# Kernel optimization log

Measured on AMD Instinct MI355X. Metric: run time of the kernel, lower is better.

## Reference

```python
import jax, jax.numpy as jnp
import numpy as np

EPS = 1e-5

def _bn(x, g, b, m, v):
    # eval-mode BatchNorm1d over channel dim of [B, C, T]
    scale = g / jnp.sqrt(v + EPS)
    return (x - m[:, None]) * scale[:, None] + b[:, None]

def _conv3(x, w, b):
    # [B, W, T] conv with kernel [W, W, 3], padding=1
    y = jax.lax.conv_general_dilated(x, w, (1,), [(1, 1)],
                                     dimension_numbers=('NCH', 'OIH', 'NCH'))
    return y + b[None, :, None]

def setup_inputs() -> dict:
    key = jax.random.key(0)
    ks = iter(jax.random.split(key, 32))
    def n(shape, s=0.05):
        return jax.random.normal(next(ks), shape, jnp.float32) * s
    def u(shape):
        return jax.random.uniform(next(ks), shape, jnp.float32, 0.5, 1.5)
    B, T, C, S, W = 128, 4096, 125, 5, 25
    return dict(
        low_freq=jax.random.normal(next(ks), (B, 10, T), jnp.float32),
        w1=n((S, W, 2)), b1=n((S, W)),
        w3=n((S - 1, W, W, 3)), b3=n((S - 1, W)),
        bn_g=jnp.ones((S, W)), bn_b=jnp.zeros((S, W)), bn_m=n((S, W)), bn_v=u((S, W)),
        gw1=n((C // 4, C)), gb1=n((C // 4,)),          # gating Linear(125, 31)
        gw2=n((S, C // 4)), gb2=n((S,)),               # gating Linear(31, 5)
        id_w=n((C, 10)), id_b=n((C,)),                 # identity_proj Conv1d(10,125,1)
        pf_w=n((C, C)), pf_b=n((C,)),                  # proj_final Conv1d(125,125,1)
        fbn_g=jnp.ones((C,)), fbn_b=jnp.zeros((C,)), fbn_m=n((C,)), fbn_v=u((C,)),
        ln_g=jnp.ones((C,)), ln_b=jnp.zeros((C,)),
        fc1_w=n((64, C)), fc1_b=n((64,)),
        fc2_w=n((2, 64)), fc2_b=n((2,)),
    )

def reference(low_freq, w1, b1, w3, b3, bn_g, bn_b, bn_m, bn_v,
              gw1, gb1, gw2, gb2, id_w, id_b, pf_w, pf_b,
              fbn_g, fbn_b, fbn_m, fbn_v, ln_g, ln_b,
              fc1_w, fc1_b, fc2_w, fc2_b):
    S = w1.shape[0]
    B, _, T = low_freq.shape
    identity = jnp.einsum('bct,oc->bot', low_freq, id_w) + id_b[None, :, None]
    chunks = low_freq.reshape(B, S, 2, T)              # torch.chunk over 10 channels
    # all 1x1 convs at once: [S, B, W, T]
    xs = jnp.einsum('bsct,swc->sbwt', chunks, w1) + b1[:, None, :, None]
    y = [None] * S
    y[S - 1] = jax.nn.relu(_bn(xs[S - 1], bn_g[S - 1], bn_b[S - 1], bn_m[S - 1], bn_v[S - 1]))
    for i in range(S - 2, -1, -1):                     # sequential Res2Net recursion
        yi = _conv3(xs[i] + y[i + 1], w3[i], b3[i])
        y[i] = jax.nn.relu(_bn(yi, bn_g[i], bn_b[i], bn_m[i], bn_v[i]))
    ms = jnp.concatenate(y, axis=1)                    # [B, 125, T]
    avg = jnp.mean(ms, axis=-1)                        # [B, 125]
    gate = jax.nn.sigmoid(jax.nn.relu(avg @ gw1.T + gb1) @ gw2.T + gb2)  # [B, S]
    yw = jnp.stack(y, axis=1) * gate[:, :, None, None] # [B, S, W, T]
    gated = yw.reshape(B, -1, T)
    proj = jnp.einsum('bct,oc->bot', gated, pf_w) + pf_b[None, :, None]
    out = jax.nn.relu(_bn(proj + identity, fbn_g, fbn_b, fbn_m, fbn_v))
    pooled = jnp.mean(out, axis=-1)                    # GAP -> [B, 125]
    mu = jnp.mean(pooled, axis=-1, keepdims=True)
    var = jnp.var(pooled, axis=-1, keepdims=True)
    normed = (pooled - mu) / jnp.sqrt(var + EPS) * ln_g + ln_b
    h = normed @ fc1_w.T + fc1_b
    h = jnp.where(h > 0, h, 0.2 * h)                   # LeakyReLU(0.2); dropout = identity (eval)
    return h @ fc2_w.T + fc2_b                         # [B, 2]
```

## Files before the change

kernel.cpp:

```cpp
#include <hip/hip_runtime.h>
#include <stdint.h>

typedef unsigned short u16;
typedef unsigned int   u32;
using short8 = __attribute__((ext_vector_type(8))) short;
using f32x4  = __attribute__((ext_vector_type(4))) float;

__device__ __forceinline__ u16 f2bf(float f){
  u32 u = __builtin_bit_cast(u32, f);
  u = u + 0x7fffu + ((u >> 16) & 1u);
  return (u16)(u >> 16);
}
__device__ __forceinline__ u32 packbf2(float a, float b){
  u32 ua = __builtin_bit_cast(u32, a) + 0x8000u;
  u32 ub = __builtin_bit_cast(u32, b) + 0x8000u;
  return (ua >> 16) | (ub & 0xffff0000u);
}

__global__ void prep_kernel(const float* __restrict__ w3,
                            const float* __restrict__ w1,
                            const float* __restrict__ b1,
                            const float* __restrict__ bng,
                            const float* __restrict__ bnv,
                            u16* __restrict__ convA)
{
  int idx = blockIdx.x*256 + threadIdx.x;
  if (idx >= 4*2*3*64*8) return;
  int j = idx & 7, l = (idx>>3) & 63, frag = idx >> 9;
  int tap = frag % 3, mt = (frag/3) & 1, lay = frag/6;
  int m = mt*16 + (l & 15);
  int k = (l>>4)*8 + j;
  float v = 0.f;
  if (m < 25){
    float a = bng[lay*25+m] * rsqrtf(bnv[lay*25+m] + 1e-5f);
    if (k < 25){
      v = a * w3[((lay*25+m)*25 + k)*3 + tap];
    } else if (k == 25){
      float s = 0.f;
      for (int c = 0; c < 25; ++c) s += w3[((lay*25+m)*25+c)*3+tap] * b1[lay*25+c];
      v = a * s;
    } else if (k <= 27){
      int e = k - 26;
      float s = 0.f;
      for (int c = 0; c < 25; ++c) s += w3[((lay*25+m)*25+c)*3+tap] * w1[(lay*25+c)*2+e];
      v = a * s;
    }
  }
  convA[idx] = f2bf(v);
}

template<int PASS, int CT>
__global__ __launch_bounds__(256, (PASS==1) ? 4 : 2)
void pass_kernel(const float* __restrict__ lfg,
                 const float* __restrict__ w1g, const float* __restrict__ b1g,
                 const float* __restrict__ b3g,
                 const float* __restrict__ bng, const float* __restrict__ bnb,
                 const float* __restrict__ bnm, const float* __restrict__ bnv,
                 const u16* __restrict__ convA, const u16* __restrict__ Ab,
                 const float* __restrict__ pfb, const float* __restrict__ idb,
                 const float* __restrict__ fbg, const float* __restrict__ fbb,
                 const float* __restrict__ fbm, const float* __restrict__ fbv,
                 float* __restrict__ outpart)
{
  constexpr int IS   = (CT-2)*16;
  constexpr int CZ   = 16*CT + 2;
  constexpr int NBLK = 4096/(4*IS);

  __shared__ __align__(16) u16 zws[4][CZ*40];
  __shared__ __align__(16) float cAs[4][32];
  __shared__ __align__(16) float w4as[32], w4bs[32], c4s[32];
  __shared__ float accC[(PASS==1)?160:4];
  __shared__ __align__(16) float AfS[(PASS==2)?128:4], BfS[(PASS==2)?128:4];

  const int tid  = threadIdx.x;
  const int lane = tid & 63, wv = tid >> 6;
  const int q = lane >> 4, c16 = lane & 15;
  const int b = blockIdx.y, blk = blockIdx.x;
  const int stripe = blk*4 + wv;
  const int tbase  = stripe*IS - 16;

  for (int x = tid; x < 4*CZ*20; x += 256) ((u32*)zws)[x] = 0u;
  __syncthreads();
  for (int x = tid; x < 4*CZ; x += 256){
    int w = x / CZ, cz = x - w*CZ;
    int t = (blk*4 + w)*IS - 16 + cz - 1;
    zws[w][cz*40 + 25] = ((unsigned)t < 4096u) ? (u16)0x3F80 : (u16)0;
  }
  if (tid < 128){
    int i = tid >> 5, ch = tid & 31;
    float cc = 0.f;
    if (ch < 25){
      float a = bng[i*25+ch]*rsqrtf(bnv[i*25+ch]+1e-5f);
      cc = (b3g[i*25+ch] - bnm[i*25+ch])*a + bnb[i*25+ch];
    }
    cAs[i][ch] = cc;
  } else if (tid < 160){
    int ch = tid - 128;
    float wa=0.f, wb=0.f, cf=0.f;
    if (ch < 25){
      float a = bng[100+ch]*rsqrtf(bnv[100+ch]+1e-5f);
      wa = a*w1g[(100+ch)*2+0]; wb = a*w1g[(100+ch)*2+1];
      cf = a*b1g[100+ch] + (bnb[100+ch] - bnm[100+ch]*a);
    }
    w4as[ch]=wa; w4bs[ch]=wb; c4s[ch]=cf;
  }
  if constexpr (PASS==1){ if (tid < 160) accC[tid] = 0.f; }
  if constexpr (PASS==2){
    if (tid < 128){
      float fs=0.f, fsh=0.f;
      if (tid < 125){
        fs  = fbg[tid]*rsqrtf(fbv[tid]+1e-5f);
        fsh = (pfb[tid]+idb[tid]-fbm[tid])*fs + fbb[tid];
      }
      AfS[tid]=fs; BfS[tid]=fsh;
    }
  }
  __syncthreads();

  u16* z = zws[wv];

  f32x4 pacc[2][8];
  if constexpr (PASS==2){
    #pragma unroll
    for (int n2=0;n2<2;++n2)
      #pragma unroll
      for (int m2=0;m2<8;++m2) pacc[n2][m2] = (f32x4){0.f,0.f,0.f,0.f};
  }

  {
    float l8[CT], l9[CT], r0[CT], r1[CT];
    #pragma unroll
    for (int ct=0; ct<CT; ++ct){
      int t = tbase + 16*ct + c16;
      bool tk = (unsigned)t < 4096u;
      l8[ct] = tk ? lfg[(b*10+8)*4096 + t] : 0.f;
      l9[ct] = tk ? lfg[(b*10+9)*4096 + t] : 0.f;
      r0[ct] = 0.f; r1[ct] = 0.f;
      if (lane < 16 && tk){
        r0[ct] = lfg[(b*10+6)*4096 + t];
        r1[ct] = lfg[(b*10+7)*4096 + t];
      }
    }
    const f32x4 wa0 = *(const f32x4*)&w4as[4*q];
    const f32x4 wa1 = *(const f32x4*)&w4as[16+4*q];
    const f32x4 wb0 = *(const f32x4*)&w4bs[4*q];
    const f32x4 wb1 = *(const f32x4*)&w4bs[16+4*q];
    const f32x4 cf0 = *(const f32x4*)&c4s[4*q];
    const f32x4 cf1 = *(const f32x4*)&c4s[16+4*q];
    float s4[8];
    #pragma unroll
    for (int e=0;e<8;++e) s4[e] = 0.f;
    #pragma unroll
    for (int ct=0; ct<CT; ++ct){
      const int lc = 16*ct + c16;
      const int t  = tbase + lc;
      const bool tok   = (unsigned)t < 4096u;
      const bool inter = (ct >= 1) && (ct <= CT-2);
      float y0[4], y1[4];
      #pragma unroll
      for (int r=0;r<4;++r){
        float a = fmaxf(wa0[r]*l8[ct] + wb0[r]*l9[ct] + cf0[r], 0.f);
        float c = fmaxf(wa1[r]*l8[ct] + wb1[r]*l9[ct] + cf1[r], 0.f);
        y0[r] = tok ? a : 0.f;
        y1[r] = tok ? c : 0.f;
        if (PASS==1 && inter){ s4[r] += y0[r]; s4[4+r] += y1[r]; }
      }
      uint2 w0; w0.x = packbf2(y0[0],y0[1]); w0.y = packbf2(y0[2],y0[3]);
      *(uint2*)&z[(lc+1)*40 + 4*q] = w0;
      if (q < 2){
        uint2 w1_; w1_.x = packbf2(y1[0],y1[1]); w1_.y = packbf2(y1[2],y1[3]);
        *(uint2*)&z[(lc+1)*40 + 16 + 4*q] = w1_;
      } else if (q == 2){
        z[(lc+1)*40 + 24] = f2bf(y1[0]);
      }
      if (lane < 16)
        *(u32*)&z[(16*ct+lane+1)*40 + 26] = packbf2(r0[ct], r1[ct]);
    }
    if constexpr (PASS==1){
      #pragma unroll
      for (int e=0;e<8;++e){
        float v = s4[e];
        v += __shfl_xor(v,1); v += __shfl_xor(v,2); v += __shfl_xor(v,4); v += __shfl_xor(v,8);
        if (c16 == 0){
          int ch = (e>>2)*16 + 4*q + (e&3);
          if (ch < 25) atomicAdd(&accC[4*32+ch], v);
        }
      }
    }
  }

  if constexpr (PASS==2){
    {
      short8 Am[8];
      #pragma unroll
      for (int m2=0;m2<8;++m2)
        Am[m2] = *(const short8*)(Ab + b*24576 + ((4*8+m2)*64 + lane)*8);
      #pragma unroll
      for (int n2=0;n2<2;++n2){
        const short8 Bm = *(const short8*)&z[(17+16*n2+c16)*40 + 8*q];
        #pragma unroll
        for (int m2=0;m2<8;++m2)
          pacc[n2][m2] = __builtin_amdgcn_mfma_f32_16x16x32_bf16(Am[m2], Bm, pacc[n2][m2],0,0,0);
      }
    }
    {
      short8 Am[8];
      #pragma unroll
      for (int m2=0;m2<8;++m2)
        Am[m2] = *(const short8*)(Ab + b*24576 + ((5*8+m2)*64 + lane)*8);
      #pragma unroll
      for (int n2=0;n2<2;++n2){
        const int t = tbase + 16 + 16*n2 + c16;
        u32 bw[4];
        #pragma unroll
        for (int p=0;p<4;++p){
          int k0 = 8*q + 2*p;
          float v0 = (k0   < 10) ? lfg[(b*10+k0  )*4096 + t] : 0.f;
          float v1 = (k0+1 < 10) ? lfg[(b*10+k0+1)*4096 + t] : 0.f;
          bw[p] = packbf2(v0, v1);
        }
        const short8 Bm = __builtin_bit_cast(short8, bw);
        #pragma unroll
        for (int m2=0;m2<8;++m2)
          pacc[n2][m2] = __builtin_amdgcn_mfma_f32_16x16x32_bf16(Am[m2], Bm, pacc[n2][m2],0,0,0);
      }
    }
  }

  for (int i = 3; i >= 0; --i){
    short8 Ac0[3], Ac1[3];
    #pragma unroll
    for (int tp=0;tp<3;++tp){
      Ac0[tp] = *(const short8*)(convA + (((i*2+0)*3+tp)*64 + lane)*8);
      Ac1[tp] = *(const short8*)(convA + (((i*2+1)*3+tp)*64 + lane)*8);
    }
    const f32x4 cc0 = *(const f32x4*)&cAs[i][4*q];
    const f32x4 cc1 = *(const f32x4*)&cAs[i][16+4*q];
    short8 Ag[8];
    if constexpr (PASS==2){
      #pragma unroll
      for (int m2=0;m2<8;++m2)
        Ag[m2] = *(const short8*)(Ab + b*24576 + ((i*8+m2)*64 + lane)*8);
    }
    float r0[CT], r1[CT];
    #pragma unroll
    for (int ct=0;ct<CT;++ct){ r0[ct]=0.f; r1[ct]=0.f; }
    if (i > 0 && lane < 16){
      #pragma unroll
      for (int ct=0;ct<CT;++ct){
        int t = tbase + 16*ct + lane;
        if ((unsigned)t < 4096u){
          r0[ct] = lfg[(b*10 + 2*i-2)*4096 + t];
          r1[ct] = lfg[(b*10 + 2*i-1)*4096 + t];
        }
      }
    }
    float ysum[8];
    #pragma unroll
    for (int e=0;e<8;++e) ysum[e] = 0.f;

    short8 F0[3], F1[3], F2[3];
    {
      const u16* p = z + c16*40 + 8*q;
      F0[0] = *(const short8*)(p);
      F0[1] = *(const short8*)(p + 40);
      F0[2] = *(const short8*)(p + 80);
      const u16* p1 = z + (16 + c16)*40 + 8*q;
      F1[0] = *(const short8*)(p1);
      F1[1] = *(const short8*)(p1 + 40);
      F1[2] = *(const short8*)(p1 + 80);
    }
    #pragma unroll
    for (int ct=0; ct<CT; ++ct){
      short8* cur = (ct%3==0) ? F0 : ((ct%3==1) ? F1 : F2);
      short8* nx2 = (ct%3==0) ? F2 : ((ct%3==1) ? F0 : F1);
      if (ct < CT-2){
        const u16* p = z + (16*(ct+2) + c16)*40 + 8*q;
        nx2[0] = *(const short8*)(p);
        nx2[1] = *(const short8*)(p + 40);
        nx2[2] = *(const short8*)(p + 80);
      }
      __builtin_amdgcn_sched_barrier(0);
      f32x4 a0 = {0.f,0.f,0.f,0.f}, a1 = {0.f,0.f,0.f,0.f};
      #pragma unroll
      for (int tp=0;tp<3;++tp){
        a0 = __builtin_amdgcn_mfma_f32_16x16x32_bf16(Ac0[tp], cur[tp], a0, 0,0,0);
        a1 = __builtin_amdgcn_mfma_f32_16x16x32_bf16(Ac1[tp], cur[tp], a1, 0,0,0);
      }
      const int lc = 16*ct + c16;
      const int t  = tbase + lc;
      const bool tok   = (unsigned)t < 4096u;
      const bool inter = (ct >= 1) && (ct <= CT-2);
      float y0[4], y1[4];
      #pragma unroll
      for (int r=0;r<4;++r){
        float u0 = fmaxf(a0[r] + cc0[r], 0.f);
        float u1 = fmaxf(a1[r] + cc1[r], 0.f);
        y0[r] = tok ? u0 : 0.f;
        y1[r] = tok ? u1 : 0.f;
        if (PASS==1 && inter){ ysum[r] += y0[r]; ysum[4+r] += y1[r]; }
      }
      if (i > 0 || PASS==2){
        uint2 w0; w0.x = packbf2(y0[0],y0[1]); w0.y = packbf2(y0[2],y0[3]);
        *(uint2*)&z[(lc+1)*40 + 4*q] = w0;
        if (q < 2){
          uint2 w1_; w1_.x = packbf2(y1[0],y1[1]); w1_.y = packbf2(y1[2],y1[3]);
          *(uint2*)&z[(lc+1)*40 + 16 + 4*q] = w1_;
        } else if (q == 2){
          z[(lc+1)*40 + 24] = f2bf(y1[0]);
        }
      }
      if (i > 0 && lane < 16)
        *(u32*)&z[(16*ct+lane+1)*40 + 26] = packbf2(r0[ct], r1[ct]);
    }
    if constexpr (PASS==1){
      #pragma unroll
      for (int e=0;e<8;++e){
        float v = ysum[e];
        v += __shfl_xor(v,1); v += __shfl_xor(v,2); v += __shfl_xor(v,4); v += __shfl_xor(v,8);
        if (c16 == 0){
          int ch = (e>>2)*16 + 4*q + (e&3);
          if (ch < 25) atomicAdd(&accC[i*32+ch], v);
        }
      }
    }
    if constexpr (PASS==2){
      #pragma unroll
      for (int n2=0;n2<2;++n2){
        const short8 Bm = *(const short8*)&z[(17+16*n2+c16)*40 + 8*q];
        #pragma unroll
        for (int m2=0;m2<8;++m2)
          pacc[n2][m2] = __builtin_amdgcn_mfma_f32_16x16x32_bf16(Ag[m2], Bm, pacc[n2][m2],0,0,0);
      }
    }
  }

  if constexpr (PASS==1){
    __syncthreads();
    if (tid < 160) outpart[(b*NBLK + blk)*160 + tid] = accC[tid];
  }
  if constexpr (PASS==2){
    f32x4 ps[8];
    #pragma unroll
    for (int m2=0;m2<8;++m2){
      const f32x4 af = *(const f32x4*)&AfS[m2*16+4*q];
      const f32x4 bf = *(const f32x4*)&BfS[m2*16+4*q];
      #pragma unroll
      for (int r=0;r<4;++r){
        float s = fmaxf(pacc[0][m2][r]*af[r] + bf[r], 0.f)
                + fmaxf(pacc[1][m2][r]*af[r] + bf[r], 0.f);
        s += __shfl_xor(s,1); s += __shfl_xor(s,2); s += __shfl_xor(s,4); s += __shfl_xor(s,8);
        ps[m2][r] = s;
      }
    }
    if (c16 == 0){
      const int widx = (b*NBLK + blk)*4 + wv;
      #pragma unroll
      for (int m2=0;m2<8;++m2)
        *(f32x4*)&outpart[widx*128 + m2*16 + 4*q] = ps[m2];
    }
  }
}

__global__ void gate_kernel(const float* __restrict__ partialC,
                            const float* __restrict__ gw1, const float* __restrict__ gb1,
                            const float* __restrict__ gw2, const float* __restrict__ gb2,
                            const float* __restrict__ pf_w, const float* __restrict__ id_w,
                            u16* __restrict__ Ab)
{
  int b = blockIdx.x, tid = threadIdx.x;
  __shared__ float avg[125], h1[31], g[6];
  if (tid < 160){
    float s = 0.f;
    for (int k = 0; k < 16; ++k) s += partialC[(b*16+k)*160 + tid];
    int sc = tid >> 5, ch = tid & 31;
    if (ch < 25) avg[sc*25+ch] = s * (1.f/4096.f);
  }
  __syncthreads();
  if (tid < 31){
    float s = gb1[tid];
    for (int c = 0; c < 125; ++c) s += avg[c] * gw1[tid*125 + c];
    h1[tid] = fmaxf(s, 0.f);
  }
  __syncthreads();
  if (tid < 5){
    float s = gb2[tid];
    for (int j = 0; j < 31; ++j) s += h1[j] * gw2[tid*31 + j];
    g[tid] = 1.f / (1.f + expf(-s));
  }
  if (tid == 5) g[5] = 1.f;
  __syncthreads();
  for (int idx = tid; idx < 24576; idx += 256){
    int j = idx & 7, l = (idx>>3) & 63, mt = (idx>>9) & 7, kt = idx >> 12;
    int m = mt*16 + (l & 15), k = (l>>4)*8 + j;
    float v = 0.f;
    if (m < 125){
      if (kt < 5){ if (k < 25) v = pf_w[m*125 + kt*25 + k] * g[kt]; }
      else       { if (k < 10) v = id_w[m*10 + k]; }
    }
    Ab[b*24576 + idx] = f2bf(v);
  }
}

__global__ void final_kernel(const float* __restrict__ pooledpart,
                             const float* __restrict__ ln_g, const float* __restrict__ ln_b,
                             const float* __restrict__ fc1_w, const float* __restrict__ fc1_b,
                             const float* __restrict__ fc2_w, const float* __restrict__ fc2_b,
                             float* __restrict__ out)
{
  int b = blockIdx.x, tid = threadIdx.x;
  __shared__ float pl[125], nr[125], hh[64], st[2];
  for (int c = tid; c < 125; c += 64){
    float s = 0.f;
    for (int k = 0; k < 128; ++k) s += pooledpart[(b*128+k)*128 + c];
    pl[c] = s * (1.f/4096.f);
  }
  __syncthreads();
  if (tid == 0){
    float mu = 0.f;
    for (int c = 0; c < 125; ++c) mu += pl[c];
    mu /= 125.f;
    float va = 0.f;
    for (int c = 0; c < 125; ++c){ float d = pl[c] - mu; va += d*d; }
    va /= 125.f;
    st[0] = mu; st[1] = rsqrtf(va + 1e-5f);
  }
  __syncthreads();
  for (int c = tid; c < 125; c += 64)
    nr[c] = (pl[c] - st[0]) * st[1] * ln_g[c] + ln_b[c];
  __syncthreads();
  {
    float s = fc1_b[tid];
    for (int c = 0; c < 125; ++c) s += nr[c] * fc1_w[tid*125 + c];
    hh[tid] = (s > 0.f) ? s : 0.2f * s;
  }
  __syncthreads();
  if (tid < 2){
    float s = fc2_b[tid];
    for (int j = 0; j < 64; ++j) s += hh[j] * fc2_w[tid*64 + j];
    out[b*2 + tid] = s;
  }
}

extern "C" void kernel_launch(void* const* d_in, const int* in_sizes, int n_in,
                              void* d_out, int out_size, void* d_ws, size_t ws_size,
                              hipStream_t stream)
{
  const float* lf    = (const float*)d_in[0];
  const float* w1    = (const float*)d_in[1];
  const float* b1    = (const float*)d_in[2];
  const float* w3    = (const float*)d_in[3];
  const float* b3    = (const float*)d_in[4];
  const float* bn_g  = (const float*)d_in[5];
  const float* bn_b  = (const float*)d_in[6];
  const float* bn_m  = (const float*)d_in[7];
  const float* bn_v  = (const float*)d_in[8];
  const float* gw1   = (const float*)d_in[9];
  const float* gb1   = (const float*)d_in[10];
  const float* gw2   = (const float*)d_in[11];
  const float* gb2   = (const float*)d_in[12];
  const float* id_w  = (const float*)d_in[13];
  const float* id_b  = (const float*)d_in[14];
  const float* pf_w  = (const float*)d_in[15];
  const float* pf_b  = (const float*)d_in[16];
  const float* fbn_g = (const float*)d_in[17];
  const float* fbn_b = (const float*)d_in[18];
  const float* fbn_m = (const float*)d_in[19];
  const float* fbn_v = (const float*)d_in[20];
  const float* ln_g  = (const float*)d_in[21];
  const float* ln_b  = (const float*)d_in[22];
  const float* fc1_w = (const float*)d_in[23];
  const float* fc1_b = (const float*)d_in[24];
  const float* fc2_w = (const float*)d_in[25];
  const float* fc2_b = (const float*)d_in[26];

  char* ws = (char*)d_ws;
  float* partialC   = (float*)ws;
  float* pooledpart = (float*)(ws + 1310720);
  u16*   Ab         = (u16*)(ws + 1310720 + 8388608);
  u16*   convA      = (u16*)(ws + 1310720 + 8388608 + 6291456);

  prep_kernel<<<48, 256, 0, stream>>>(w3, w1, b1, bn_g, bn_v, convA);
  pass_kernel<1,6><<<dim3(16,128), 256, 0, stream>>>(lf, w1, b1, b3, bn_g, bn_b,
      bn_m, bn_v, convA, Ab, pf_b, id_b, fbn_g, fbn_b, fbn_m, fbn_v, partialC);
  gate_kernel<<<128, 256, 0, stream>>>(partialC, gw1, gb1, gw2, gb2, pf_w, id_w, Ab);
  pass_kernel<2,4><<<dim3(32,128), 256, 0, stream>>>(lf, w1, b1, b3, bn_g, bn_b,
      bn_m, bn_v, convA, Ab, pf_b, id_b, fbn_g, fbn_b, fbn_m, fbn_v, pooledpart);
  final_kernel<<<128, 64, 0, stream>>>(pooledpart, ln_g, ln_b, fc1_w, fc1_b,
      fc2_w, fc2_b, (float*)d_out);
}
```

Baseline: 357.4 us.

## Unify pass kernels on 32-wide stripes with ping-pong LDS buffers

Both passes now use a fixed 64-column window per wave, so pass 1 shrinks from 6 to 4 column tiles and runs on twice as many blocks with lower occupancy bounds. Each wave gets two LDS buffers, so each recursion level reads one buffer and writes the other instead of overwriting in place. The low-frequency input pairs are loaded once up front into packed registers rather than reloaded each level. The goal is to cut redundant halo compute, repeated global loads and in-place hazards, at the cost of more halo overhead per useful column in pass 1 and doubled LDS.

```diff
diff --git a/kernel.cpp b/kernel.cpp
--- a/kernel.cpp
+++ b/kernel.cpp
@@ -49,8 +49,8 @@
   convA[idx] = f2bf(v);
 }
 
-template<int PASS, int CT>
-__global__ __launch_bounds__(256, (PASS==1) ? 4 : 2)
+template<int PASS>
+__global__ __launch_bounds__(256, (PASS==1) ? 3 : 2)
 void pass_kernel(const float* __restrict__ lfg,
                  const float* __restrict__ w1g, const float* __restrict__ b1g,
                  const float* __restrict__ b3g,
@@ -62,11 +62,8 @@
                  const float* __restrict__ fbm, const float* __restrict__ fbv,
                  float* __restrict__ outpart)
 {
-  constexpr int IS   = (CT-2)*16;
-  constexpr int CZ   = 16*CT + 2;
-  constexpr int NBLK = 4096/(4*IS);
-
-  __shared__ __align__(16) u16 zws[4][CZ*40];
+  constexpr int CZ = 66;
+  __shared__ __align__(16) u16 zws[4][2][CZ*40];
   __shared__ __align__(16) float cAs[4][32];
   __shared__ __align__(16) float w4as[32], w4bs[32], c4s[32];
   __shared__ float accC[(PASS==1)?160:4];
@@ -76,15 +73,15 @@
   const int lane = tid & 63, wv = tid >> 6;
   const int q = lane >> 4, c16 = lane & 15;
   const int b = blockIdx.y, blk = blockIdx.x;
-  const int stripe = blk*4 + wv;
-  const int tbase  = stripe*IS - 16;
-
-  for (int x = tid; x < 4*CZ*20; x += 256) ((u32*)zws)[x] = 0u;
-  __syncthreads();
-  for (int x = tid; x < 4*CZ; x += 256){
-    int w = x / CZ, cz = x - w*CZ;
-    int t = (blk*4 + w)*IS - 16 + cz - 1;
-    zws[w][cz*40 + 25] = ((unsigned)t < 4096u) ? (u16)0x3F80 : (u16)0;
+  const int s = blk*4 + wv;
+  const int tbase = s*32 - 16;
+
+  for (int x = tid; x < 4*2*CZ*20; x += 256) ((u32*)zws)[x] = 0u;
+  __syncthreads();
+  for (int x = tid; x < 4*2*CZ; x += 256){
+    int w = x/(2*CZ), rb = (x/CZ)&1, cz = x%CZ;
+    int t = (blk*4+w)*32 - 16 + cz - 1;
+    zws[w][rb][cz*40 + 25] = ((unsigned)t < 4096u) ? (u16)0x3F80 : (u16)0;
   }
   if (tid < 128){
     int i = tid >> 5, ch = tid & 31;
@@ -117,7 +114,19 @@
   }
   __syncthreads();
 
-  u16* z = zws[wv];
+  const float* lfb = lfg + b*10*4096;
+
+  u32 lpair[4];
+  {
+    int t = tbase + lane;
+    bool ok = (unsigned)t < 4096u;
+    #pragma unroll
+    for (int k = 0; k < 4; ++k){
+      float a = ok ? lfb[(2*k  )*4096 + t] : 0.f;
+      float c = ok ? lfb[(2*k+1)*4096 + t] : 0.f;
+      lpair[k] = packbf2(a, c);
+    }
+  }
 
   f32x4 pacc[2][8];
   if constexpr (PASS==2){
@@ -127,20 +136,9 @@
       for (int m2=0;m2<8;++m2) pacc[n2][m2] = (f32x4){0.f,0.f,0.f,0.f};
   }
 
+  u16* bufA = zws[wv][0];
+
   {
-    float l8[CT], l9[CT], r0[CT], r1[CT];
-    #pragma unroll
-    for (int ct=0; ct<CT; ++ct){
-      int t = tbase + 16*ct + c16;
-      bool tk = (unsigned)t < 4096u;
-      l8[ct] = tk ? lfg[(b*10+8)*4096 + t] : 0.f;
-      l9[ct] = tk ? lfg[(b*10+9)*4096 + t] : 0.f;
-      r0[ct] = 0.f; r1[ct] = 0.f;
-      if (lane < 16 && tk){
-        r0[ct] = lfg[(b*10+6)*4096 + t];
-        r1[ct] = lfg[(b*10+7)*4096 + t];
-      }
-    }
     const f32x4 wa0 = *(const f32x4*)&w4as[4*q];
     const f32x4 wa1 = *(const f32x4*)&w4as[16+4*q];
     const f32x4 wb0 = *(const f32x4*)&w4bs[4*q];
@@ -151,31 +149,34 @@
     #pragma unroll
     for (int e=0;e<8;++e) s4[e] = 0.f;
     #pragma unroll
-    for (int ct=0; ct<CT; ++ct){
-      const int lc = 16*ct + c16;
-      const int t  = tbase + lc;
-      const bool tok   = (unsigned)t < 4096u;
-      const bool inter = (ct >= 1) && (ct <= CT-2);
+    for (int ct=0; ct<4; ++ct){
+      const int wc = 16*ct + c16;
+      const int t  = tbase + wc;
+      const bool tok = (unsigned)t < 4096u;
+      const float l8 = tok ? lfb[8*4096 + t] : 0.f;
+      const float l9 = tok ? lfb[9*4096 + t] : 0.f;
       float y0[4], y1[4];
       #pragma unroll
       for (int r=0;r<4;++r){
-        float a = fmaxf(wa0[r]*l8[ct] + wb0[r]*l9[ct] + cf0[r], 0.f);
-        float c = fmaxf(wa1[r]*l8[ct] + wb1[r]*l9[ct] + cf1[r], 0.f);
+        float a = fmaxf(wa0[r]*l8 + wb0[r]*l9 + cf0[r], 0.f);
+        float c = fmaxf(wa1[r]*l8 + wb1[r]*l9 + cf1[r], 0.f);
         y0[r] = tok ? a : 0.f;
         y1[r] = tok ? c : 0.f;
-        if (PASS==1 && inter){ s4[r] += y0[r]; s4[4+r] += y1[r]; }
+      }
+      if (PASS==1 && (ct==1 || ct==2)){
+        #pragma unroll
+        for (int r=0;r<4;++r){ s4[r] += y0[r]; s4[4+r] += y1[r]; }
       }
       uint2 w0; w0.x = packbf2(y0[0],y0[1]); w0.y = packbf2(y0[2],y0[3]);
-      *(uint2*)&z[(lc+1)*40 + 4*q] = w0;
+      *(uint2*)&bufA[(wc+1)*40 + 4*q] = w0;
       if (q < 2){
         uint2 w1_; w1_.x = packbf2(y1[0],y1[1]); w1_.y = packbf2(y1[2],y1[3]);
-        *(uint2*)&z[(lc+1)*40 + 16 + 4*q] = w1_;
+        *(uint2*)&bufA[(wc+1)*40 + 16 + 4*q] = w1_;
       } else if (q == 2){
-        z[(lc+1)*40 + 24] = f2bf(y1[0]);
-      }
-      if (lane < 16)
-        *(u32*)&z[(16*ct+lane+1)*40 + 26] = packbf2(r0[ct], r1[ct]);
-    }
+        bufA[(wc+1)*40 + 24] = f2bf(y1[0]);
+      }
+    }
+    *(u32*)&bufA[(lane+1)*40 + 26] = lpair[3];
     if constexpr (PASS==1){
       #pragma unroll
       for (int e=0;e<8;++e){
@@ -197,7 +198,7 @@
         Am[m2] = *(const short8*)(Ab + b*24576 + ((4*8+m2)*64 + lane)*8);
       #pragma unroll
       for (int n2=0;n2<2;++n2){
-        const short8 Bm = *(const short8*)&z[(17+16*n2+c16)*40 + 8*q];
+        const short8 Bm = *(const short8*)&bufA[(17+16*n2+c16)*40 + 8*q];
         #pragma unroll
         for (int m2=0;m2<8;++m2)
           pacc[n2][m2] = __builtin_amdgcn_mfma_f32_16x16x32_bf16(Am[m2], Bm, pacc[n2][m2],0,0,0);
@@ -215,8 +216,8 @@
         #pragma unroll
         for (int p=0;p<4;++p){
           int k0 = 8*q + 2*p;
-          float v0 = (k0   < 10) ? lfg[(b*10+k0  )*4096 + t] : 0.f;
-          float v1 = (k0+1 < 10) ? lfg[(b*10+k0+1)*4096 + t] : 0.f;
+          float v0 = (k0   < 10) ? lfb[k0*4096 + t] : 0.f;
+          float v1 = (k0+1 < 10) ? lfb[(k0+1)*4096 + t] : 0.f;
           bw[p] = packbf2(v0, v1);
         }
         const short8 Bm = __builtin_bit_cast(short8, bw);
@@ -227,7 +228,10 @@
     }
   }
 
+  #pragma unroll
   for (int i = 3; i >= 0; --i){
+    u16* src = zws[wv][(3-i)&1];
+    u16* dst = zws[wv][(4-i)&1];
     short8 Ac0[3], Ac1[3];
     #pragma unroll
     for (int tp=0;tp<3;++tp){
@@ -236,61 +240,26 @@
     }
     const f32x4 cc0 = *(const f32x4*)&cAs[i][4*q];
     const f32x4 cc1 = *(const f32x4*)&cAs[i][16+4*q];
-    short8 Ag[8];
-    if constexpr (PASS==2){
-      #pragma unroll
-      for (int m2=0;m2<8;++m2)
-        Ag[m2] = *(const short8*)(Ab + b*24576 + ((i*8+m2)*64 + lane)*8);
-    }
-    float r0[CT], r1[CT];
-    #pragma unroll
-    for (int ct=0;ct<CT;++ct){ r0[ct]=0.f; r1[ct]=0.f; }
-    if (i > 0 && lane < 16){
-      #pragma unroll
-      for (int ct=0;ct<CT;++ct){
-        int t = tbase + 16*ct + lane;
-        if ((unsigned)t < 4096u){
-          r0[ct] = lfg[(b*10 + 2*i-2)*4096 + t];
-          r1[ct] = lfg[(b*10 + 2*i-1)*4096 + t];
-        }
-      }
-    }
     float ysum[8];
     #pragma unroll
     for (int e=0;e<8;++e) ysum[e] = 0.f;
 
-    short8 F0[3], F1[3], F2[3];
-    {
-      const u16* p = z + c16*40 + 8*q;
-      F0[0] = *(const short8*)(p);
-      F0[1] = *(const short8*)(p + 40);
-      F0[2] = *(const short8*)(p + 80);
-      const u16* p1 = z + (16 + c16)*40 + 8*q;
-      F1[0] = *(const short8*)(p1);
-      F1[1] = *(const short8*)(p1 + 40);
-      F1[2] = *(const short8*)(p1 + 80);
-    }
-    #pragma unroll
-    for (int ct=0; ct<CT; ++ct){
-      short8* cur = (ct%3==0) ? F0 : ((ct%3==1) ? F1 : F2);
-      short8* nx2 = (ct%3==0) ? F2 : ((ct%3==1) ? F0 : F1);
-      if (ct < CT-2){
-        const u16* p = z + (16*(ct+2) + c16)*40 + 8*q;
-        nx2[0] = *(const short8*)(p);
-        nx2[1] = *(const short8*)(p + 40);
-        nx2[2] = *(const short8*)(p + 80);
-      }
-      __builtin_amdgcn_sched_barrier(0);
+    #pragma unroll
+    for (int ct=0; ct<4; ++ct){
+      const int wc = 16*ct + c16;
+      const u16* p = src + wc*40 + 8*q;
+      short8 t0 = *(const short8*)(p);
+      short8 t1 = *(const short8*)(p + 40);
+      short8 t2 = *(const short8*)(p + 80);
       f32x4 a0 = {0.f,0.f,0.f,0.f}, a1 = {0.f,0.f,0.f,0.f};
-      #pragma unroll
-      for (int tp=0;tp<3;++tp){
-        a0 = __builtin_amdgcn_mfma_f32_16x16x32_bf16(Ac0[tp], cur[tp], a0, 0,0,0);
-        a1 = __builtin_amdgcn_mfma_f32_16x16x32_bf16(Ac1[tp], cur[tp], a1, 0,0,0);
-      }
-      const int lc = 16*ct + c16;
-      const int t  = tbase + lc;
-      const bool tok   = (unsigned)t < 4096u;
-      const bool inter = (ct >= 1) && (ct <= CT-2);
+      a0 = __builtin_amdgcn_mfma_f32_16x16x32_bf16(Ac0[0], t0, a0, 0,0,0);
+      a1 = __builtin_amdgcn_mfma_f32_16x16x32_bf16(Ac1[0], t0, a1, 0,0,0);
+      a0 = __builtin_amdgcn_mfma_f32_16x16x32_bf16(Ac0[1], t1, a0, 0,0,0);
+      a1 = __builtin_amdgcn_mfma_f32_16x16x32_bf16(Ac1[1], t1, a1, 0,0,0);
+      a0 = __builtin_amdgcn_mfma_f32_16x16x32_bf16(Ac0[2], t2, a0, 0,0,0);
+      a1 = __builtin_amdgcn_mfma_f32_16x16x32_bf16(Ac1[2], t2, a1, 0,0,0);
+      const int t = tbase + wc;
+      const bool tok = (unsigned)t < 4096u;
       float y0[4], y1[4];
       #pragma unroll
       for (int r=0;r<4;++r){
@@ -298,21 +267,21 @@
         float u1 = fmaxf(a1[r] + cc1[r], 0.f);
         y0[r] = tok ? u0 : 0.f;
         y1[r] = tok ? u1 : 0.f;
-        if (PASS==1 && inter){ ysum[r] += y0[r]; ysum[4+r] += y1[r]; }
-      }
-      if (i > 0 || PASS==2){
-        uint2 w0; w0.x = packbf2(y0[0],y0[1]); w0.y = packbf2(y0[2],y0[3]);
-        *(uint2*)&z[(lc+1)*40 + 4*q] = w0;
-        if (q < 2){
-          uint2 w1_; w1_.x = packbf2(y1[0],y1[1]); w1_.y = packbf2(y1[2],y1[3]);
-          *(uint2*)&z[(lc+1)*40 + 16 + 4*q] = w1_;
-        } else if (q == 2){
-          z[(lc+1)*40 + 24] = f2bf(y1[0]);
-        }
-      }
-      if (i > 0 && lane < 16)
-        *(u32*)&z[(16*ct+lane+1)*40 + 26] = packbf2(r0[ct], r1[ct]);
-    }
+      }
+      if (PASS==1 && (ct==1 || ct==2)){
+        #pragma unroll
+        for (int r=0;r<4;++r){ ysum[r] += y0[r]; ysum[4+r] += y1[r]; }
+      }
+      uint2 w0; w0.x = packbf2(y0[0],y0[1]); w0.y = packbf2(y0[2],y0[3]);
+      *(uint2*)&dst[(wc+1)*40 + 4*q] = w0;
+      if (q < 2){
+        uint2 w1_; w1_.x = packbf2(y1[0],y1[1]); w1_.y = packbf2(y1[2],y1[3]);
+        *(uint2*)&dst[(wc+1)*40 + 16 + 4*q] = w1_;
+      } else if (q == 2){
+        dst[(wc+1)*40 + 24] = f2bf(y1[0]);
+      }
+    }
+    if (i > 0) *(u32*)&dst[(lane+1)*40 + 26] = lpair[i-1];
     if constexpr (PASS==1){
       #pragma unroll
       for (int e=0;e<8;++e){
@@ -325,19 +294,23 @@
       }
     }
     if constexpr (PASS==2){
+      short8 Am[8];
+      #pragma unroll
+      for (int m2=0;m2<8;++m2)
+        Am[m2] = *(const short8*)(Ab + b*24576 + ((i*8+m2)*64 + lane)*8);
       #pragma unroll
       for (int n2=0;n2<2;++n2){
-        const short8 Bm = *(const short8*)&z[(17+16*n2+c16)*40 + 8*q];
+        const short8 Bm = *(const short8*)&dst[(17+16*n2+c16)*40 + 8*q];
         #pragma unroll
         for (int m2=0;m2<8;++m2)
-          pacc[n2][m2] = __builtin_amdgcn_mfma_f32_16x16x32_bf16(Ag[m2], Bm, pacc[n2][m2],0,0,0);
+          pacc[n2][m2] = __builtin_amdgcn_mfma_f32_16x16x32_bf16(Am[m2], Bm, pacc[n2][m2],0,0,0);
       }
     }
   }
 
   if constexpr (PASS==1){
     __syncthreads();
-    if (tid < 160) outpart[(b*NBLK + blk)*160 + tid] = accC[tid];
+    if (tid < 160) outpart[(b*32 + blk)*160 + tid] = accC[tid];
   }
   if constexpr (PASS==2){
     f32x4 ps[8];
@@ -347,14 +320,14 @@
       const f32x4 bf = *(const f32x4*)&BfS[m2*16+4*q];
       #pragma unroll
       for (int r=0;r<4;++r){
-        float s = fmaxf(pacc[0][m2][r]*af[r] + bf[r], 0.f)
-                + fmaxf(pacc[1][m2][r]*af[r] + bf[r], 0.f);
-        s += __shfl_xor(s,1); s += __shfl_xor(s,2); s += __shfl_xor(s,4); s += __shfl_xor(s,8);
-        ps[m2][r] = s;
+        float s2 = fmaxf(pacc[0][m2][r]*af[r] + bf[r], 0.f)
+                 + fmaxf(pacc[1][m2][r]*af[r] + bf[r], 0.f);
+        s2 += __shfl_xor(s2,1); s2 += __shfl_xor(s2,2); s2 += __shfl_xor(s2,4); s2 += __shfl_xor(s2,8);
+        ps[m2][r] = s2;
       }
     }
     if (c16 == 0){
-      const int widx = (b*NBLK + blk)*4 + wv;
+      const int widx = (b*32 + blk)*4 + wv;
       #pragma unroll
       for (int m2=0;m2<8;++m2)
         *(f32x4*)&outpart[widx*128 + m2*16 + 4*q] = ps[m2];
@@ -372,7 +345,7 @@
   __shared__ float avg[125], h1[31], g[6];
   if (tid < 160){
     float s = 0.f;
-    for (int k = 0; k < 16; ++k) s += partialC[(b*16+k)*160 + tid];
+    for (int k = 0; k < 32; ++k) s += partialC[(b*32+k)*160 + tid];
     int sc = tid >> 5, ch = tid & 31;
     if (ch < 25) avg[sc*25+ch] = s * (1.f/4096.f);
   }
@@ -476,15 +449,15 @@
 
   char* ws = (char*)d_ws;
   float* partialC   = (float*)ws;
-  float* pooledpart = (float*)(ws + 1310720);
-  u16*   Ab         = (u16*)(ws + 1310720 + 8388608);
-  u16*   convA      = (u16*)(ws + 1310720 + 8388608 + 6291456);
+  float* pooledpart = (float*)(ws + 2621440);
+  u16*   Ab         = (u16*)(ws + 2621440 + 8388608);
+  u16*   convA      = (u16*)(ws + 2621440 + 8388608 + 6291456);
 
   prep_kernel<<<48, 256, 0, stream>>>(w3, w1, b1, bn_g, bn_v, convA);
-  pass_kernel<1,6><<<dim3(16,128), 256, 0, stream>>>(lf, w1, b1, b3, bn_g, bn_b,
+  pass_kernel<1><<<dim3(32,128), 256, 0, stream>>>(lf, w1, b1, b3, bn_g, bn_b,
       bn_m, bn_v, convA, Ab, pf_b, id_b, fbn_g, fbn_b, fbn_m, fbn_v, partialC);
   gate_kernel<<<128, 256, 0, stream>>>(partialC, gw1, gb1, gw2, gb2, pf_w, id_w, Ab);
-  pass_kernel<2,4><<<dim3(32,128), 256, 0, stream>>>(lf, w1, b1, b3, bn_g, bn_b,
+  pass_kernel<2><<<dim3(32,128), 256, 0, stream>>>(lf, w1, b1, b3, bn_g, bn_b,
       bn_m, bn_v, convA, Ab, pf_b, id_b, fbn_g, fbn_b, fbn_m, fbn_v, pooledpart);
   final_kernel<<<128, 64, 0, stream>>>(pooledpart, ln_g, ln_b, fc1_w, fc1_b,
       fc2_w, fc2_b, (float*)d_out);
```

After: 397.2 us. 11.1% more time.
